# Kernel optimization log

Measured on AMD Instinct MI355X. Metric: run time of the kernel, lower is better.

The kernel has to match this reference:

```python
import jax, jax.numpy as jnp
import numpy as np

NB = 4096      # num_batch
NUM = 128      # trajectory samples (P rows)
NVAR = 16      # polynomial coeffs (P cols)
NOBS = 10      # obstacles
NL, NU = 4, 8  # num_lower, num_upper
NPART = NU - NL
T_FIN = 10.0
A_OBS, B_OBS = 6.0, 3.2
RHO_INEQ = RHO_OBS = RHO_LANE = 1.0
V_MIN, V_MAX, A_MAX = 0.1, 30.0, 18.0
MAXITER = 30
W_SM = 100.0


def setup_inputs() -> dict:
    key = jax.random.key(0)
    ks = jax.random.split(key, 13)
    f = jnp.float32
    return {
        'P': jax.random.normal(ks[0], (NUM, NVAR), f),
        'Pdot': jax.random.normal(ks[1], (NUM, NVAR), f),
        'Pddot': jax.random.normal(ks[2], (NUM, NVAR), f),
        'init_state_ego': jax.random.normal(ks[3], (NB, 4), f),
        'fin_state_ego': jax.random.normal(ks[4], (NB, 3), f),
        'closest_obs': jax.random.normal(ks[5], (NB, 2 * NOBS), f),
        'v_obs': jax.random.normal(ks[6], (NB, 2 * NOBS), f),
        'y_ub': jax.random.uniform(ks[7], (NB,), f),
        'y_lb': jax.random.normal(ks[8], (NB,), f),
        'lamda_x': jax.random.normal(ks[9], (NB, NVAR), f),
        'lamda_y': jax.random.normal(ks[10], (NB, NVAR), f),
        'c_x_partial': jax.random.normal(ks[11], (NB, NPART), f),
        'c_y_partial': jax.random.normal(ks[12], (NB, NPART), f),
    }


def _forward(P, Pdot, Pddot, init_state_ego, fin_state_ego, closest_obs, v_obs,
             y_ub, y_lb, lamda_x, lamda_y, c_x_partial, c_y_partial):
    num, nvar = P.shape
    tot_time = jnp.linspace(0.0, T_FIN, num)
    eye = jnp.eye(nvar, dtype=P.dtype)
    A_part = eye[NL:NU]
    A_eq_x = jnp.vstack([P[0], Pdot[0], Pddot[0], Pdot[-1], A_part])            # [4+NPART, nvar]
    A_eq_y = jnp.vstack([P[0], Pdot[0], Pddot[0], P[-1], Pdot[-1], A_part])     # [5+NPART, nvar]
    cost_sm = W_SM * (Pddot.T @ Pddot + 0.1 * eye)
    A_vel, A_acc = Pdot, Pddot
    A_obs_mat = jnp.tile(P, (NOBS, 1))            # [NOBS*num, nvar]
    A_lane = jnp.vstack([P, -P])                  # [2*num, nvar]

    def kkt_inv(cost, A_eq):
        m = A_eq.shape[0]
        top = jnp.hstack([cost, A_eq.T])
        bot = jnp.hstack([A_eq, jnp.zeros((m, m), cost.dtype)])
        return jnp.linalg.inv(jnp.vstack([top, bot]))

    # --- obstacle trajectories: [B, NOBS*num] ---
    x_obs = closest_obs[:, :NOBS]; y_obs = closest_obs[:, NOBS:2 * NOBS]
    vx_obs = v_obs[:, :NOBS];      vy_obs = v_obs[:, NOBS:2 * NOBS]
    x_obs_traj = (x_obs[:, :, None] + vx_obs[:, :, None] * tot_time).reshape(NB, NOBS * num)
    y_obs_traj = (y_obs[:, :, None] + vy_obs[:, :, None] * tot_time).reshape(NB, NOBS * num)

    # --- boundary vectors ---
    x_init = init_state_ego[:, 0:1]; y_init = init_state_ego[:, 1:2]
    v_init = init_state_ego[:, 2:3]; psi_init = init_state_ego[:, 3:4]
    vx_init = v_init * jnp.cos(psi_init); vy_init = v_init * jnp.sin(psi_init)
    zc = jnp.zeros((NB, 1), P.dtype)
    x_fin = fin_state_ego[:, 0:1]; y_fin = fin_state_ego[:, 1:2]
    vx_fin = jnp.clip(fin_state_ego[:, 2:3], V_MIN, V_MAX)  # computed as in original (unused in b_eq)
    b_eq_x = jnp.hstack([x_init, vx_init, zc, x_fin, c_x_partial])
    b_eq_y = jnp.hstack([y_init, vy_init, zc, y_fin, zc, c_y_partial])

    # --- initialization QP (lincost = 0) ---
    cmi_x0 = kkt_inv(cost_sm, A_eq_x)
    cmi_y0 = kkt_inv(cost_sm, A_eq_y)
    sol_x0 = jnp.hstack([jnp.zeros((NB, nvar), P.dtype), b_eq_x]) @ cmi_x0.T
    sol_y0 = jnp.hstack([jnp.zeros((NB, nvar), P.dtype), b_eq_y]) @ cmi_y0.T
    primal_sol = jnp.hstack([sol_x0[:, :nvar], sol_y0[:, :nvar]])

    # --- optimizer KKT inverses ---
    cost_x = cost_sm + RHO_INEQ * (A_acc.T @ A_acc) + RHO_INEQ * (A_vel.T @ A_vel) + RHO_OBS * (A_obs_mat.T @ A_obs_mat)
    cost_y = cost_x + RHO_LANE * (A_lane.T @ A_lane)
    cmi_x = kkt_inv(cost_x, A_eq_x)
    cmi_y = kkt_inv(cost_y, A_eq_y)

    ones_num = jnp.ones((NB, num), P.dtype)
    b_lane = jnp.hstack([y_ub[:, None] * ones_num, -y_lb[:, None] * ones_num])  # [B, 2*num]

    def step(carry, _):
        primal, lx, ly = carry
        cx, cy = primal[:, :nvar], primal[:, nvar:]
        x, xdot, xddot = cx @ P.T, cx @ Pdot.T, cx @ Pddot.T      # [B, num]
        y, ydot, yddot = cy @ P.T, cy @ Pdot.T, cy @ Pddot.T

        wc = jnp.tile(x, (1, NOBS)) - x_obs_traj                   # [B, NOBS*num]
        ws = jnp.tile(y, (1, NOBS)) - y_obs_traj
        alpha_obs = jnp.arctan2(ws * A_OBS, wc * B_OBS)
        co, so = jnp.cos(alpha_obs), jnp.sin(alpha_obs)
        c1 = RHO_OBS * (A_OBS ** 2 * co ** 2 + B_OBS ** 2 * so ** 2)
        c2 = RHO_OBS * (A_OBS * wc * co + B_OBS * ws * so)
        d_obs = jnp.maximum(1.0, c2 / c1)

        alpha_v = jnp.arctan2(ydot, xdot)
        cv, sv = jnp.cos(alpha_v), jnp.sin(alpha_v)
        d_v = jnp.clip(RHO_INEQ * (xdot * cv + ydot * sv) / (RHO_INEQ * (cv ** 2 + sv ** 2)), V_MIN, V_MAX)

        alpha_a = jnp.arctan2(yddot, xddot)
        ca, sa = jnp.cos(alpha_a), jnp.sin(alpha_a)
        d_a = jnp.clip(RHO_INEQ * (xddot * ca + yddot * sa) / (RHO_INEQ * (ca ** 2 + sa ** 2)), 0.0, A_MAX)

        Ay = cy @ A_lane.T                                         # [B, 2*num]
        s_lane = jnp.maximum(0.0, -Ay + b_lane)
        res_lane = Ay - b_lane + s_lane
        res_ax, res_ay = xddot - d_a * ca, yddot - d_a * sa
        res_vx, res_vy = xdot - d_v * cv, ydot - d_v * sv
        res_xo, res_yo = wc - A_OBS * d_obs * co, ws - B_OBS * d_obs * so

        lx = lx - RHO_INEQ * (res_ax @ A_acc) - RHO_INEQ * (res_vx @ A_vel) - RHO_OBS * (res_xo @ A_obs_mat)
        ly = ly - RHO_INEQ * (res_ay @ A_acc) - RHO_INEQ * (res_vy @ A_vel) \
                - RHO_OBS * (res_yo @ A_obs_mat) - RHO_LANE * (res_lane @ A_lane)

        tmp_xo = x_obs_traj + A_OBS * d_obs * co
        tmp_yo = y_obs_traj + B_OBS * d_obs * so
        lincost_x = -lx - RHO_OBS * (tmp_xo @ A_obs_mat) - RHO_INEQ * ((d_a * ca) @ A_acc) - RHO_INEQ * ((d_v * cv) @ A_vel)
        lincost_y = -ly - RHO_OBS * (tmp_yo @ A_obs_mat) - RHO_INEQ * ((d_a * sa) @ A_acc) - RHO_INEQ * ((d_v * sv) @ A_vel) \
                    - RHO_LANE * ((b_lane - s_lane) @ A_lane)
        sol_x = jnp.hstack([-lincost_x, b_eq_x]) @ cmi_x.T
        sol_y = jnp.hstack([-lincost_y, b_eq_y]) @ cmi_y.T
        primal = jnp.hstack([sol_x[:, :nvar], sol_y[:, :nvar]])
        return (primal, lx, ly), None

    (primal_sol, lamda_x, lamda_y), _ = jax.lax.scan(step, (primal_sol, lamda_x, lamda_y), None, length=MAXITER)
    return primal_sol


def reference(P, Pdot, Pddot, init_state_ego, fin_state_ego, closest_obs, v_obs,
              y_ub, y_lb, lamda_x, lamda_y, c_x_partial, c_y_partial):
    return _forward(P, Pdot, Pddot, init_state_ego, fin_state_ego, closest_obs, v_obs,
                    y_ub, y_lb, lamda_x, lamda_y, c_x_partial, c_y_partial)
```

## Files before the change

kernel.cpp:

```cpp
#include <hip/hip_runtime.h>
#include <math.h>

#define NBATCH 4096
#define TNUM   128
#define NOBSC  10
#define MAXIT  30

#define WS_MX   0
#define WS_MY   256
#define WS_MGX  512
#define WS_MGY  768
#define WS_NX   1024
#define WS_NY   1152
#define WS_NX0  1296
#define WS_NY0  1424

#define RSTRIDE 132

union F4 { float4 v; float f[4]; };

__global__ __launch_bounds__(64) void planner_setup(
    const float* __restrict__ P, const float* __restrict__ Pd, const float* __restrict__ Pdd,
    float* __restrict__ ws)
{
  const int mid = blockIdx.x;
  const int tid = threadIdx.x;
  __shared__ double C[16][16];
  __shared__ double G[16][16];
  __shared__ double Ae[9][16];
  __shared__ double aug[25][50];
  __shared__ int pivs;

  const bool isY = (mid & 1);
  const int  m   = isY ? 9 : 8;
  const int  n   = 16 + m;
  const int  w   = 2 * n;

  for (int e = tid; e < 256; e += 64) {
    const int j = e >> 4, k = e & 15;
    double gdd = 0.0, gd = 0.0, g0 = 0.0;
    for (int t = 0; t < TNUM; ++t) {
      gdd += (double)Pdd[t*16+j] * (double)Pdd[t*16+k];
      gd  += (double)Pd [t*16+j] * (double)Pd [t*16+k];
      g0  += (double)P  [t*16+j] * (double)P  [t*16+k];
    }
    const double cs = 100.0 * (gdd + ((j == k) ? 0.1 : 0.0));
    const double g  = gdd + gd + (isY ? 12.0 : 10.0) * g0;
    G[j][k] = g;
    C[j][k] = (mid >= 2) ? (cs + g) : cs;
  }
  if (tid < 16) {
    const int j = tid;
    Ae[0][j] = (double)P  [0*16+j];
    Ae[1][j] = (double)Pd [0*16+j];
    Ae[2][j] = (double)Pdd[0*16+j];
    if (!isY) {
      Ae[3][j] = (double)Pd[127*16+j];
      for (int r = 4; r < 8; ++r) Ae[r][j] = (j == r) ? 1.0 : 0.0;
    } else {
      Ae[3][j] = (double)P [127*16+j];
      Ae[4][j] = (double)Pd[127*16+j];
      for (int r = 5; r < 9; ++r) Ae[r][j] = (j == (r-1)) ? 1.0 : 0.0;
    }
  }
  __syncthreads();

  for (int e = tid; e < n * w; e += 64) {
    const int r = e / w, c = e % w;
    double val;
    if (c < n) {
      if (r < 16) val = (c < 16) ? C[r][c] : Ae[c-16][r];
      else        val = (c < 16) ? Ae[r-16][c] : 0.0;
    } else {
      val = ((c - n) == r) ? 1.0 : 0.0;
    }
    aug[r][c] = val;
  }
  __syncthreads();

  for (int k = 0; k < n; ++k) {
    if (tid == 0) {
      int p = k; double best = fabs(aug[k][k]);
      for (int r = k+1; r < n; ++r) { double a = fabs(aug[r][k]); if (a > best) { best = a; p = r; } }
      pivs = p;
    }
    __syncthreads();
    const int p = pivs;
    if (p != k) {
      for (int c = tid; c < w; c += 64) { double t = aug[k][c]; aug[k][c] = aug[p][c]; aug[p][c] = t; }
    }
    __syncthreads();
    const double ipiv = 1.0 / aug[k][k];
    for (int c = tid; c < w; c += 64) aug[k][c] *= ipiv;
    __syncthreads();
    for (int r = tid; r < n; r += 64) {
      if (r != k) {
        const double f = aug[r][k];
        for (int c = k; c < w; ++c) aug[r][c] -= f * aug[k][c];
      }
    }
    __syncthreads();
  }

  if (mid == 0) {
    for (int e = tid; e < 16*8; e += 64) ws[WS_NX0 + e] = (float)aug[e >> 3][n + 16 + (e & 7)];
  } else if (mid == 1) {
    for (int e = tid; e < 16*9; e += 64) ws[WS_NY0 + e] = (float)aug[e / 9][n + 16 + (e % 9)];
  } else if (mid == 2) {
    for (int e = tid; e < 256;  e += 64) ws[WS_MX + e] = (float)aug[e >> 4][n + (e & 15)];
    for (int e = tid; e < 16*8; e += 64) ws[WS_NX + e] = (float)aug[e >> 3][n + 16 + (e & 7)];
  } else {
    for (int e = tid; e < 256;  e += 64) ws[WS_MY + e] = (float)aug[e >> 4][n + (e & 15)];
    for (int e = tid; e < 16*9; e += 64) ws[WS_NY + e] = (float)aug[e / 9][n + 16 + (e % 9)];
  }

  if (mid >= 2) {
    for (int e = tid; e < 256; e += 64) {
      const int j = e >> 4, k = e & 15;
      double s = 0.0;
      for (int mm = 0; mm < 16; ++mm) s += aug[j][n + mm] * G[mm][k];
      ws[(mid == 2 ? WS_MGX : WS_MGY) + e] = (float)s;
    }
  }
}

__global__ __launch_bounds__(128) void planner_main(
    const float* __restrict__ P, const float* __restrict__ Pd, const float* __restrict__ Pdd,
    const float* __restrict__ init_state, const float* __restrict__ fin_state,
    const float* __restrict__ cobs, const float* __restrict__ vobs,
    const float* __restrict__ yub_g, const float* __restrict__ ylb_g,
    const float* __restrict__ lamx_g, const float* __restrict__ lamy_g,
    const float* __restrict__ cxp_g, const float* __restrict__ cyp_g,
    const float* __restrict__ ws, float* __restrict__ out)
{
  const int b    = blockIdx.x;
  const int tid  = threadIdx.x;
  const int lane = tid & 63;
  const int wv   = tid >> 6;
  const int r32  = lane & 31;
  const int rr   = tid & 15;
  const int side = (tid >> 4) & 1;

  __shared__ alignas(16) float red[32*RSTRIDE];
  __shared__ alignas(16) float cLw[2][32];
  __shared__ alignas(16) float hLw[2][32];
  __shared__ float pL[2][32];

  float Pr[16], Pdr[16], Pddr[16];
  #pragma unroll
  for (int q = 0; q < 4; ++q) {
    const float4 a  = *reinterpret_cast<const float4*>(P   + tid*16 + 4*q);
    const float4 bb = *reinterpret_cast<const float4*>(Pd  + tid*16 + 4*q);
    const float4 cc = *reinterpret_cast<const float4*>(Pdd + tid*16 + 4*q);
    Pr  [4*q+0]=a.x;  Pr  [4*q+1]=a.y;  Pr  [4*q+2]=a.z;  Pr  [4*q+3]=a.w;
    Pdr [4*q+0]=bb.x; Pdr [4*q+1]=bb.y; Pdr [4*q+2]=bb.z; Pdr [4*q+3]=bb.w;
    Pddr[4*q+0]=cc.x; Pddr[4*q+1]=cc.y; Pddr[4*q+2]=cc.z; Pddr[4*q+3]=cc.w;
  }

  float xot32[10], yot6[10];
  {
    const float tt = (float)tid * (10.0f/127.0f);
    #pragma unroll
    for (int oo = 0; oo < NOBSC; ++oo) {
      xot32[oo] = 3.2f * fmaf(vobs[b*20+oo],      tt, cobs[b*20+oo]);
      yot6 [oo] = 6.0f * fmaf(vobs[b*20+10+oo],   tt, cobs[b*20+10+oo]);
    }
  }
  const float yub = yub_g[b], ylb = ylb_g[b];

  float lam, constv, myc;
  {
    float beq[9];
    const float vi  = init_state[b*4+2];
    const float psi = init_state[b*4+3];
    if (side == 0) {
      beq[0] = init_state[b*4+0];
      beq[1] = vi * cosf(psi);
      beq[2] = 0.f;
      beq[3] = fin_state[b*3+0];
      #pragma unroll
      for (int i2 = 0; i2 < 4; ++i2) beq[4+i2] = cxp_g[b*4+i2];
      beq[8] = 0.f;
    } else {
      beq[0] = init_state[b*4+1];
      beq[1] = vi * sinf(psi);
      beq[2] = 0.f;
      beq[3] = fin_state[b*3+1];
      beq[4] = 0.f;
      #pragma unroll
      for (int i2 = 0; i2 < 4; ++i2) beq[5+i2] = cyp_g[b*4+i2];
    }
    const int nstr = side ? 9 : 8;
    const float* Np  = ws + (side ? WS_NY  : WS_NX ) + rr*nstr;
    const float* N0p = ws + (side ? WS_NY0 : WS_NX0) + rr*nstr;
    float cv = 0.f, c0 = 0.f;
    #pragma unroll
    for (int mm = 0; mm < 9; ++mm) {
      const float bm = beq[mm];
      cv = fmaf(Np[mm],  bm, cv);
      c0 = fmaf(N0p[mm], bm, c0);
    }
    constv = cv;
    myc    = c0;
    lam = (side == 0) ? lamx_g[b*16 + rr] : lamy_g[b*16 + rr];
    if (lane < 32) cLw[wv][lane] = c0;
  }

  const float* Mrow  = ws + (side ? WS_MY  : WS_MX ) + rr*16;
  const float* MGrow = ws + (side ? WS_MGY : WS_MGX) + rr*16;

  #pragma unroll 1
  for (int it = 0; it < MAXIT; ++it) {
    float x=0.f, y=0.f, xd=0.f, yd=0.f, xdd=0.f, ydd=0.f;
    #pragma unroll
    for (int q = 0; q < 4; ++q) {
      F4 cx4, cy4;
      cx4.v = *reinterpret_cast<const float4*>(&cLw[wv][4*q]);
      cy4.v = *reinterpret_cast<const float4*>(&cLw[wv][16 + 4*q]);
      #pragma unroll
      for (int j = 0; j < 4; ++j) {
        const int jj = 4*q + j;
        const float cc = cx4.f[j], dd = cy4.f[j];
        x   = fmaf(Pr  [jj], cc, x);   y   = fmaf(Pr  [jj], dd, y);
        xd  = fmaf(Pdr [jj], cc, xd);  yd  = fmaf(Pdr [jj], dd, yd);
        xdd = fmaf(Pddr[jj], cc, xdd); ydd = fmaf(Pddr[jj], dd, ydd);
      }
    }

    const float ria = rsqrtf(fmaxf(fmaf(xdd, xdd, ydd*ydd), 1e-36f));
    const float ga1 = 1.0f - fminf(1.0f, 18.0f * ria);
    const float riv = rsqrtf(fmaxf(fmaf(xd, xd, yd*yd), 1e-36f));
    const float gv1 = 1.0f - fminf(fmaxf(1.0f, 0.1f*riv), 30.0f*riv);

    float Sxp = 0.f, Syp = 0.f;
    #pragma unroll
    for (int oo = 0; oo < NOBSC; ++oo) {
      const float bw = fmaf(3.2f, x, -xot32[oo]);
      const float aw = fmaf(6.0f, y, -yot6[oo]);
      const float ri = rsqrtf(fmaxf(fmaf(bw, bw, aw*aw), 1e-36f));
      const float e  = fmaxf(fmaf(19.2f, ri, -1.0f), 0.f);
      Sxp = fmaf(e, bw, Sxp);
      Syp = fmaf(e, aw, Syp);
    }
    const float c0p = -Sxp * 0.3125f;
    const float rln = fmaxf(y - yub, 0.f) - fmaxf(ylb - y, 0.f);
    const float c2p = rln - Syp * (1.0f/6.0f);
    const float c0dd = xdd * ga1, c0d = xd * gv1;
    const float c2dd = ydd * ga1, c2d = yd * gv1;

    {
      float* col = red + tid;
      #pragma unroll
      for (int j = 0; j < 16; ++j) {
        col[j*RSTRIDE]      = fmaf(c0dd, Pddr[j], fmaf(c0d, Pdr[j], c0p * Pr[j]));
        col[(16+j)*RSTRIDE] = fmaf(c2dd, Pddr[j], fmaf(c2d, Pdr[j], c2p * Pr[j]));
      }
    }
    __syncthreads();

    {
      const int qq = tid >> 5;
      const float* rb = red + r32*RSTRIDE + qq*32;
      float s0=0.f, s1=0.f, s2=0.f, s3=0.f;
      #pragma unroll
      for (int mch = 0; mch < 8; ++mch) {
        const float4 t = *reinterpret_cast<const float4*>(rb + 4*mch);
        s0 += t.x; s1 += t.y; s2 += t.z; s3 += t.w;
      }
      float s = (s0 + s1) + (s2 + s3);
      s += __shfl_xor(s, 32);
      if (lane < 32) pL[wv][lane] = s;
      __syncthreads();

      const float S = s + pL[wv ^ 1][r32];
      lam -= S;
      const float h = lam - S;
      if (lane < 32) hLw[wv][lane] = h;
    }

    {
      float acc = constv;
      #pragma unroll
      for (int q = 0; q < 4; ++q) {
        F4 m4, g4, h4, c4;
        m4.v = *reinterpret_cast<const float4*>(Mrow  + 4*q);
        g4.v = *reinterpret_cast<const float4*>(MGrow + 4*q);
        h4.v = *reinterpret_cast<const float4*>(&hLw[wv][side*16 + 4*q]);
        c4.v = *reinterpret_cast<const float4*>(&cLw[wv][side*16 + 4*q]);
        #pragma unroll
        for (int j = 0; j < 4; ++j)
          acc = fmaf(g4.f[j], c4.f[j], fmaf(m4.f[j], h4.f[j], acc));
      }
      myc = acc;
      if (lane < 32) cLw[wv][lane] = acc;
    }
  }

  if (tid < 32) out[b*32 + tid] = myc;
}

extern "C" void kernel_launch(void* const* d_in, const int* in_sizes, int n_in,
                              void* d_out, int out_size, void* d_ws, size_t ws_size,
                              hipStream_t stream) {
  const float* P    = (const float*)d_in[0];
  const float* Pd   = (const float*)d_in[1];
  const float* Pdd  = (const float*)d_in[2];
  const float* init = (const float*)d_in[3];
  const float* fin  = (const float*)d_in[4];
  const float* cobs = (const float*)d_in[5];
  const float* vobs = (const float*)d_in[6];
  const float* yub  = (const float*)d_in[7];
  const float* ylb  = (const float*)d_in[8];
  const float* lamx = (const float*)d_in[9];
  const float* lamy = (const float*)d_in[10];
  const float* cxp  = (const float*)d_in[11];
  const float* cyp  = (const float*)d_in[12];
  float* ws  = (float*)d_ws;
  float* o   = (float*)d_out;

  planner_setup<<<dim3(4), dim3(64), 0, stream>>>(P, Pd, Pdd, ws);
  planner_main<<<dim3(NBATCH), dim3(128), 0, stream>>>(
      P, Pd, Pdd, init, fin, cobs, vobs, yub, ylb, lamx, lamy, cxp, cyp, ws, o);
}
```

Before: 246.1 us.

## Run each batch on a single wavefront with packed FMA and DPP reductions

The main kernel now uses one 64-thread wavefront per batch instead of two, with each thread handling two trajectory samples. __syncthreads is replaced by wave barriers. Packed 2-wide FMAs are used for the polynomial evaluations and obstacle terms, and the 32-row projection reduction is done with DPP quad sums followed by a much smaller shared buffer. This removes block-level barriers and most LDS traffic, but doubles per-thread work and register pressure and adds select logic.

```diff
diff --git a/kernel.cpp b/kernel.cpp
--- a/kernel.cpp
+++ b/kernel.cpp
@@ -15,9 +15,22 @@
 #define WS_NX0  1296
 #define WS_NY0  1424
 
-#define RSTRIDE 132
-
+#define RS 36
+
+typedef float f32x2 __attribute__((ext_vector_type(2)));
 union F4 { float4 v; float f[4]; };
+
+__device__ __forceinline__ f32x2 pfma(f32x2 a, f32x2 b, f32x2 c) {
+  return __builtin_elementwise_fma(a, b, c);
+}
+
+__device__ __forceinline__ float qsum(float v) {
+  float s = v + __int_as_float(__builtin_amdgcn_update_dpp(
+      0, __float_as_int(v), 0xB1, 0xF, 0xF, true));
+  s = s + __int_as_float(__builtin_amdgcn_update_dpp(
+      0, __float_as_int(s), 0x4E, 0xF, 0xF, true));
+  return s;
+}
 
 __global__ __launch_bounds__(64) void planner_setup(
     const float* __restrict__ P, const float* __restrict__ Pd, const float* __restrict__ Pdd,
@@ -37,17 +50,17 @@
   const int  w   = 2 * n;
 
   for (int e = tid; e < 256; e += 64) {
-    const int j = e >> 4, k = e & 15;
+    const int j = e >> 4, kk = e & 15;
     double gdd = 0.0, gd = 0.0, g0 = 0.0;
     for (int t = 0; t < TNUM; ++t) {
-      gdd += (double)Pdd[t*16+j] * (double)Pdd[t*16+k];
-      gd  += (double)Pd [t*16+j] * (double)Pd [t*16+k];
-      g0  += (double)P  [t*16+j] * (double)P  [t*16+k];
-    }
-    const double cs = 100.0 * (gdd + ((j == k) ? 0.1 : 0.0));
+      gdd += (double)Pdd[t*16+j] * (double)Pdd[t*16+kk];
+      gd  += (double)Pd [t*16+j] * (double)Pd [t*16+kk];
+      g0  += (double)P  [t*16+j] * (double)P  [t*16+kk];
+    }
+    const double cs = 100.0 * (gdd + ((j == kk) ? 0.1 : 0.0));
     const double g  = gdd + gd + (isY ? 12.0 : 10.0) * g0;
-    G[j][k] = g;
-    C[j][k] = (mid >= 2) ? (cs + g) : cs;
+    G[j][kk] = g;
+    C[j][kk] = (mid >= 2) ? (cs + g) : cs;
   }
   if (tid < 16) {
     const int j = tid;
@@ -78,25 +91,25 @@
   }
   __syncthreads();
 
-  for (int k = 0; k < n; ++k) {
+  for (int kk = 0; kk < n; ++kk) {
     if (tid == 0) {
-      int p = k; double best = fabs(aug[k][k]);
-      for (int r = k+1; r < n; ++r) { double a = fabs(aug[r][k]); if (a > best) { best = a; p = r; } }
+      int p = kk; double best = fabs(aug[kk][kk]);
+      for (int r = kk+1; r < n; ++r) { double a = fabs(aug[r][kk]); if (a > best) { best = a; p = r; } }
       pivs = p;
     }
     __syncthreads();
     const int p = pivs;
-    if (p != k) {
-      for (int c = tid; c < w; c += 64) { double t = aug[k][c]; aug[k][c] = aug[p][c]; aug[p][c] = t; }
+    if (p != kk) {
+      for (int c = tid; c < w; c += 64) { double t = aug[kk][c]; aug[kk][c] = aug[p][c]; aug[p][c] = t; }
     }
     __syncthreads();
-    const double ipiv = 1.0 / aug[k][k];
-    for (int c = tid; c < w; c += 64) aug[k][c] *= ipiv;
+    const double ipiv = 1.0 / aug[kk][kk];
+    for (int c = tid; c < w; c += 64) aug[kk][c] *= ipiv;
     __syncthreads();
     for (int r = tid; r < n; r += 64) {
-      if (r != k) {
-        const double f = aug[r][k];
-        for (int c = k; c < w; ++c) aug[r][c] -= f * aug[k][c];
+      if (r != kk) {
+        const double f = aug[r][kk];
+        for (int c = kk; c < w; ++c) aug[r][c] -= f * aug[kk][c];
       }
     }
     __syncthreads();
@@ -116,15 +129,15 @@
 
   if (mid >= 2) {
     for (int e = tid; e < 256; e += 64) {
-      const int j = e >> 4, k = e & 15;
+      const int j = e >> 4, kk = e & 15;
       double s = 0.0;
-      for (int mm = 0; mm < 16; ++mm) s += aug[j][n + mm] * G[mm][k];
+      for (int mm = 0; mm < 16; ++mm) s += aug[j][n + mm] * G[mm][kk];
       ws[(mid == 2 ? WS_MGX : WS_MGY) + e] = (float)s;
     }
   }
 }
 
-__global__ __launch_bounds__(128) void planner_main(
+__global__ __launch_bounds__(64) void planner_main(
     const float* __restrict__ P, const float* __restrict__ Pd, const float* __restrict__ Pdd,
     const float* __restrict__ init_state, const float* __restrict__ fin_state,
     const float* __restrict__ cobs, const float* __restrict__ vobs,
@@ -135,40 +148,55 @@
 {
   const int b    = blockIdx.x;
   const int tid  = threadIdx.x;
-  const int lane = tid & 63;
-  const int wv   = tid >> 6;
-  const int r32  = lane & 31;
+  const int o32  = tid & 31;
+  const int cc   = tid >> 5;
   const int rr   = tid & 15;
   const int side = (tid >> 4) & 1;
-
-  __shared__ alignas(16) float red[32*RSTRIDE];
-  __shared__ alignas(16) float cLw[2][32];
-  __shared__ alignas(16) float hLw[2][32];
-  __shared__ float pL[2][32];
-
-  float Pr[16], Pdr[16], Pddr[16];
+  const int q4   = tid >> 2;
+  const int k    = tid & 3;
+
+  __shared__ alignas(16) float red[16*RS];
+  __shared__ alignas(16) float cL[32];
+  __shared__ alignas(16) float hL[32];
+
+  f32x2 Pr2[2][8], Pdr2[2][8], Pddr2[2][8];
   #pragma unroll
-  for (int q = 0; q < 4; ++q) {
-    const float4 a  = *reinterpret_cast<const float4*>(P   + tid*16 + 4*q);
-    const float4 bb = *reinterpret_cast<const float4*>(Pd  + tid*16 + 4*q);
-    const float4 cc = *reinterpret_cast<const float4*>(Pdd + tid*16 + 4*q);
-    Pr  [4*q+0]=a.x;  Pr  [4*q+1]=a.y;  Pr  [4*q+2]=a.z;  Pr  [4*q+3]=a.w;
-    Pdr [4*q+0]=bb.x; Pdr [4*q+1]=bb.y; Pdr [4*q+2]=bb.z; Pdr [4*q+3]=bb.w;
-    Pddr[4*q+0]=cc.x; Pddr[4*q+1]=cc.y; Pddr[4*q+2]=cc.z; Pddr[4*q+3]=cc.w;
-  }
-
-  float xot32[10], yot6[10];
+  for (int u = 0; u < 2; ++u) {
+    const int t = tid + 64*u;
+    #pragma unroll
+    for (int q = 0; q < 4; ++q) {
+      F4 a, bb, ce;
+      a.v  = *reinterpret_cast<const float4*>(P   + t*16 + 4*q);
+      bb.v = *reinterpret_cast<const float4*>(Pd  + t*16 + 4*q);
+      ce.v = *reinterpret_cast<const float4*>(Pdd + t*16 + 4*q);
+      Pr2  [u][2*q+0] = f32x2{a.f[0],  a.f[1]};  Pr2  [u][2*q+1] = f32x2{a.f[2],  a.f[3]};
+      Pdr2 [u][2*q+0] = f32x2{bb.f[0], bb.f[1]}; Pdr2 [u][2*q+1] = f32x2{bb.f[2], bb.f[3]};
+      Pddr2[u][2*q+0] = f32x2{ce.f[0], ce.f[1]}; Pddr2[u][2*q+1] = f32x2{ce.f[2], ce.f[3]};
+    }
+  }
+
+  f32x2 xot0[5], yot0[5], xot1[5], yot1[5];
   {
-    const float tt = (float)tid * (10.0f/127.0f);
+    const float tt0 = (float)tid        * (10.0f/127.0f);
+    const float tt1 = (float)(tid + 64) * (10.0f/127.0f);
     #pragma unroll
-    for (int oo = 0; oo < NOBSC; ++oo) {
-      xot32[oo] = 3.2f * fmaf(vobs[b*20+oo],      tt, cobs[b*20+oo]);
-      yot6 [oo] = 6.0f * fmaf(vobs[b*20+10+oo],   tt, cobs[b*20+10+oo]);
+    for (int o5 = 0; o5 < 5; ++o5) {
+      const int o = 2*o5;
+      const float xo0 = cobs[b*20+o],    xo1 = cobs[b*20+o+1];
+      const float yo0 = cobs[b*20+10+o], yo1 = cobs[b*20+11+o];
+      const float vx0 = vobs[b*20+o],    vx1 = vobs[b*20+o+1];
+      const float vy0 = vobs[b*20+10+o], vy1 = vobs[b*20+11+o];
+      xot0[o5] = f32x2{3.2f*fmaf(vx0,tt0,xo0), 3.2f*fmaf(vx1,tt0,xo1)};
+      yot0[o5] = f32x2{6.0f*fmaf(vy0,tt0,yo0), 6.0f*fmaf(vy1,tt0,yo1)};
+      xot1[o5] = f32x2{3.2f*fmaf(vx0,tt1,xo0), 3.2f*fmaf(vx1,tt1,xo1)};
+      yot1[o5] = f32x2{6.0f*fmaf(vy0,tt1,yo0), 6.0f*fmaf(vy1,tt1,yo1)};
     }
   }
   const float yub = yub_g[b], ylb = ylb_g[b];
 
-  float lam, constv, myc;
+  float lam = (o32 < 16) ? lamx_g[b*16 + o32] : lamy_g[b*16 + (o32 - 16)];
+
+  float constv, myc;
   {
     float beq[9];
     const float vi  = init_state[b*4+2];
@@ -202,98 +230,148 @@
     }
     constv = cv;
     myc    = c0;
-    lam = (side == 0) ? lamx_g[b*16 + rr] : lamy_g[b*16 + rr];
-    if (lane < 32) cLw[wv][lane] = c0;
-  }
+  }
+  if (tid < 32) cL[tid] = myc;
 
   const float* Mrow  = ws + (side ? WS_MY  : WS_MX ) + rr*16;
   const float* MGrow = ws + (side ? WS_MGY : WS_MGX) + rr*16;
+  const bool  kb2 = (k & 2) != 0;
+  const int   k1  = k & 1;
 
   #pragma unroll 1
   for (int it = 0; it < MAXIT; ++it) {
-    float x=0.f, y=0.f, xd=0.f, yd=0.f, xdd=0.f, ydd=0.f;
+    __builtin_amdgcn_wave_barrier();
+    f32x2 xv0{},yv0{},xdv0{},ydv0{},xddv0{},yddv0{};
+    f32x2 xv1{},yv1{},xdv1{},ydv1{},xddv1{},yddv1{};
     #pragma unroll
     for (int q = 0; q < 4; ++q) {
       F4 cx4, cy4;
-      cx4.v = *reinterpret_cast<const float4*>(&cLw[wv][4*q]);
-      cy4.v = *reinterpret_cast<const float4*>(&cLw[wv][16 + 4*q]);
-      #pragma unroll
-      for (int j = 0; j < 4; ++j) {
-        const int jj = 4*q + j;
-        const float cc = cx4.f[j], dd = cy4.f[j];
-        x   = fmaf(Pr  [jj], cc, x);   y   = fmaf(Pr  [jj], dd, y);
-        xd  = fmaf(Pdr [jj], cc, xd);  yd  = fmaf(Pdr [jj], dd, yd);
-        xdd = fmaf(Pddr[jj], cc, xdd); ydd = fmaf(Pddr[jj], dd, ydd);
+      cx4.v = *reinterpret_cast<const float4*>(&cL[4*q]);
+      cy4.v = *reinterpret_cast<const float4*>(&cL[16 + 4*q]);
+      const f32x2 c01 = f32x2{cx4.f[0], cx4.f[1]}, c23 = f32x2{cx4.f[2], cx4.f[3]};
+      const f32x2 d01 = f32x2{cy4.f[0], cy4.f[1]}, d23 = f32x2{cy4.f[2], cy4.f[3]};
+      xv0   = pfma(Pr2  [0][2*q], c01, xv0);   xv0   = pfma(Pr2  [0][2*q+1], c23, xv0);
+      yv0   = pfma(Pr2  [0][2*q], d01, yv0);   yv0   = pfma(Pr2  [0][2*q+1], d23, yv0);
+      xdv0  = pfma(Pdr2 [0][2*q], c01, xdv0);  xdv0  = pfma(Pdr2 [0][2*q+1], c23, xdv0);
+      ydv0  = pfma(Pdr2 [0][2*q], d01, ydv0);  ydv0  = pfma(Pdr2 [0][2*q+1], d23, ydv0);
+      xddv0 = pfma(Pddr2[0][2*q], c01, xddv0); xddv0 = pfma(Pddr2[0][2*q+1], c23, xddv0);
+      yddv0 = pfma(Pddr2[0][2*q], d01, yddv0); yddv0 = pfma(Pddr2[0][2*q+1], d23, yddv0);
+      xv1   = pfma(Pr2  [1][2*q], c01, xv1);   xv1   = pfma(Pr2  [1][2*q+1], c23, xv1);
+      yv1   = pfma(Pr2  [1][2*q], d01, yv1);   yv1   = pfma(Pr2  [1][2*q+1], d23, yv1);
+      xdv1  = pfma(Pdr2 [1][2*q], c01, xdv1);  xdv1  = pfma(Pdr2 [1][2*q+1], c23, xdv1);
+      ydv1  = pfma(Pdr2 [1][2*q], d01, ydv1);  ydv1  = pfma(Pdr2 [1][2*q+1], d23, ydv1);
+      xddv1 = pfma(Pddr2[1][2*q], c01, xddv1); xddv1 = pfma(Pddr2[1][2*q+1], c23, xddv1);
+      yddv1 = pfma(Pddr2[1][2*q], d01, yddv1); yddv1 = pfma(Pddr2[1][2*q+1], d23, yddv1);
+    }
+    const float x0=xv0.x+xv0.y, y0=yv0.x+yv0.y, xd0=xdv0.x+xdv0.y, yd0=ydv0.x+ydv0.y;
+    const float xdd0=xddv0.x+xddv0.y, ydd0=yddv0.x+yddv0.y;
+    const float x1=xv1.x+xv1.y, y1=yv1.x+yv1.y, xd1=xdv1.x+xdv1.y, yd1=ydv1.x+ydv1.y;
+    const float xdd1=xddv1.x+xddv1.y, ydd1=yddv1.x+yddv1.y;
+
+    const float ria0 = rsqrtf(fmaxf(fmaf(xdd0,xdd0,ydd0*ydd0), 1e-36f));
+    const float ga10 = 1.0f - fminf(1.0f, 18.0f*ria0);
+    const float riv0 = rsqrtf(fmaxf(fmaf(xd0,xd0,yd0*yd0), 1e-36f));
+    const float gv10 = 1.0f - fminf(fmaxf(1.0f, 0.1f*riv0), 30.0f*riv0);
+    const float ria1 = rsqrtf(fmaxf(fmaf(xdd1,xdd1,ydd1*ydd1), 1e-36f));
+    const float ga11 = 1.0f - fminf(1.0f, 18.0f*ria1);
+    const float riv1 = rsqrtf(fmaxf(fmaf(xd1,xd1,yd1*yd1), 1e-36f));
+    const float gv11 = 1.0f - fminf(fmaxf(1.0f, 0.1f*riv1), 30.0f*riv1);
+
+    f32x2 Sx0{}, Sy0{}, Sx1{}, Sy1{};
+    {
+      const f32x2 xb0 = f32x2{3.2f*x0, 3.2f*x0}, yb0 = f32x2{6.0f*y0, 6.0f*y0};
+      const f32x2 xb1 = f32x2{3.2f*x1, 3.2f*x1}, yb1 = f32x2{6.0f*y1, 6.0f*y1};
+      #pragma unroll
+      for (int o5 = 0; o5 < 5; ++o5) {
+        const f32x2 bw0 = xb0 - xot0[o5], aw0 = yb0 - yot0[o5];
+        const f32x2 bw1 = xb1 - xot1[o5], aw1 = yb1 - yot1[o5];
+        const f32x2 r20 = pfma(bw0,bw0,aw0*aw0);
+        const f32x2 r21 = pfma(bw1,bw1,aw1*aw1);
+        const f32x2 ee0 = f32x2{
+          fmaxf(fmaf(19.2f, rsqrtf(fmaxf(r20.x,1e-36f)), -1.0f), 0.f),
+          fmaxf(fmaf(19.2f, rsqrtf(fmaxf(r20.y,1e-36f)), -1.0f), 0.f)};
+        const f32x2 ee1 = f32x2{
+          fmaxf(fmaf(19.2f, rsqrtf(fmaxf(r21.x,1e-36f)), -1.0f), 0.f),
+          fmaxf(fmaf(19.2f, rsqrtf(fmaxf(r21.y,1e-36f)), -1.0f), 0.f)};
+        Sx0 = pfma(ee0, bw0, Sx0);  Sy0 = pfma(ee0, aw0, Sy0);
+        Sx1 = pfma(ee1, bw1, Sx1);  Sy1 = pfma(ee1, aw1, Sy1);
       }
     }
-
-    const float ria = rsqrtf(fmaxf(fmaf(xdd, xdd, ydd*ydd), 1e-36f));
-    const float ga1 = 1.0f - fminf(1.0f, 18.0f * ria);
-    const float riv = rsqrtf(fmaxf(fmaf(xd, xd, yd*yd), 1e-36f));
-    const float gv1 = 1.0f - fminf(fmaxf(1.0f, 0.1f*riv), 30.0f*riv);
-
-    float Sxp = 0.f, Syp = 0.f;
+    const float c0p0 = -(Sx0.x+Sx0.y)*0.3125f;
+    const float rln0 = fmaxf(y0-yub,0.f) - fmaxf(ylb-y0,0.f);
+    const float c2p0 = rln0 - (Sy0.x+Sy0.y)*(1.0f/6.0f);
+    const float c0dd0 = xdd0*ga10, c0d0 = xd0*gv10;
+    const float c2dd0 = ydd0*ga10, c2d0 = yd0*gv10;
+    const float c0p1 = -(Sx1.x+Sx1.y)*0.3125f;
+    const float rln1 = fmaxf(y1-yub,0.f) - fmaxf(ylb-y1,0.f);
+    const float c2p1 = rln1 - (Sy1.x+Sy1.y)*(1.0f/6.0f);
+    const float c0dd1 = xdd1*ga11, c0d1 = xd1*gv11;
+    const float c2dd1 = ydd1*ga11, c2d1 = yd1*gv11;
+
+    float outv[8];
     #pragma unroll
-    for (int oo = 0; oo < NOBSC; ++oo) {
-      const float bw = fmaf(3.2f, x, -xot32[oo]);
-      const float aw = fmaf(6.0f, y, -yot6[oo]);
-      const float ri = rsqrtf(fmaxf(fmaf(bw, bw, aw*aw), 1e-36f));
-      const float e  = fmaxf(fmaf(19.2f, ri, -1.0f), 0.f);
-      Sxp = fmaf(e, bw, Sxp);
-      Syp = fmaf(e, aw, Syp);
-    }
-    const float c0p = -Sxp * 0.3125f;
-    const float rln = fmaxf(y - yub, 0.f) - fmaxf(ylb - y, 0.f);
-    const float c2p = rln - Syp * (1.0f/6.0f);
-    const float c0dd = xdd * ga1, c0d = xd * gv1;
-    const float c2dd = ydd * ga1, c2d = yd * gv1;
-
+    for (int s2 = 0; s2 < 8; ++s2) outv[s2] = 0.f;
     {
-      float* col = red + tid;
-      #pragma unroll
-      for (int j = 0; j < 16; ++j) {
-        col[j*RSTRIDE]      = fmaf(c0dd, Pddr[j], fmaf(c0d, Pdr[j], c0p * Pr[j]));
-        col[(16+j)*RSTRIDE] = fmaf(c2dd, Pddr[j], fmaf(c2d, Pdr[j], c2p * Pr[j]));
+      const f32x2 A00{c0dd0,c0dd0}, D00{c0d0,c0d0}, Q00{c0p0,c0p0};
+      const f32x2 A20{c2dd0,c2dd0}, D20{c2d0,c2d0}, Q20{c2p0,c2p0};
+      const f32x2 A01{c0dd1,c0dd1}, D01{c0d1,c0d1}, Q01{c0p1,c0p1};
+      const f32x2 A21{c2dd1,c2dd1}, D21{c2d1,c2d1}, Q21{c2p1,c2p1};
+      #pragma unroll
+      for (int j2 = 0; j2 < 8; ++j2) {
+        f32x2 vx = pfma(A00, Pddr2[0][j2], pfma(D00, Pdr2[0][j2], Q00*Pr2[0][j2]));
+        vx = pfma(A01, Pddr2[1][j2], pfma(D01, Pdr2[1][j2], pfma(Q01, Pr2[1][j2], vx)));
+        f32x2 vy = pfma(A20, Pddr2[0][j2], pfma(D20, Pdr2[0][j2], Q20*Pr2[0][j2]));
+        vy = pfma(A21, Pddr2[1][j2], pfma(D21, Pdr2[1][j2], pfma(Q21, Pr2[1][j2], vy)));
+        const float qx0 = qsum(vx.x), qx1 = qsum(vx.y);
+        const float qy0 = qsum(vy.x), qy1 = qsum(vy.y);
+        const float s0 = kb2 ? qy0 : qx0;
+        const float s1 = kb2 ? qy1 : qx1;
+        const bool match = (k1 == (j2 >> 2));
+        const int  sb = 2*(j2 & 3);
+        outv[sb]   = match ? s0 : outv[sb];
+        outv[sb+1] = match ? s1 : outv[sb+1];
       }
     }
-    __syncthreads();
-
+    __builtin_amdgcn_wave_barrier();
     {
-      const int qq = tid >> 5;
-      const float* rb = red + r32*RSTRIDE + qq*32;
-      float s0=0.f, s1=0.f, s2=0.f, s3=0.f;
-      #pragma unroll
-      for (int mch = 0; mch < 8; ++mch) {
-        const float4 t = *reinterpret_cast<const float4*>(rb + 4*mch);
-        s0 += t.x; s1 += t.y; s2 += t.z; s3 += t.w;
-      }
-      float s = (s0 + s1) + (s2 + s3);
+      float* wr = red + q4*RS + 8*k;
+      *reinterpret_cast<float4*>(wr)     = float4{outv[0],outv[1],outv[2],outv[3]};
+      *reinterpret_cast<float4*>(wr + 4) = float4{outv[4],outv[5],outv[6],outv[7]};
+    }
+    __builtin_amdgcn_wave_barrier();
+
+    float h;
+    {
+      const float* rd = red + (cc*8)*RS + o32;
+      float s = 0.f;
+      #pragma unroll
+      for (int i = 0; i < 8; ++i) s += rd[i*RS];
       s += __shfl_xor(s, 32);
-      if (lane < 32) pL[wv][lane] = s;
-      __syncthreads();
-
-      const float S = s + pL[wv ^ 1][r32];
-      lam -= S;
-      const float h = lam - S;
-      if (lane < 32) hLw[wv][lane] = h;
-    }
+      lam -= s;
+      h = lam - s;
+    }
+    __builtin_amdgcn_wave_barrier();
+    if (tid < 32) hL[tid] = h;
+    __builtin_amdgcn_wave_barrier();
 
     {
-      float acc = constv;
+      f32x2 accv{};
       #pragma unroll
       for (int q = 0; q < 4; ++q) {
         F4 m4, g4, h4, c4;
         m4.v = *reinterpret_cast<const float4*>(Mrow  + 4*q);
         g4.v = *reinterpret_cast<const float4*>(MGrow + 4*q);
-        h4.v = *reinterpret_cast<const float4*>(&hLw[wv][side*16 + 4*q]);
-        c4.v = *reinterpret_cast<const float4*>(&cLw[wv][side*16 + 4*q]);
-        #pragma unroll
-        for (int j = 0; j < 4; ++j)
-          acc = fmaf(g4.f[j], c4.f[j], fmaf(m4.f[j], h4.f[j], acc));
+        h4.v = *reinterpret_cast<const float4*>(&hL[side*16 + 4*q]);
+        c4.v = *reinterpret_cast<const float4*>(&cL[side*16 + 4*q]);
+        accv = pfma(f32x2{m4.f[0],m4.f[1]}, f32x2{h4.f[0],h4.f[1]}, accv);
+        accv = pfma(f32x2{g4.f[0],g4.f[1]}, f32x2{c4.f[0],c4.f[1]}, accv);
+        accv = pfma(f32x2{m4.f[2],m4.f[3]}, f32x2{h4.f[2],h4.f[3]}, accv);
+        accv = pfma(f32x2{g4.f[2],g4.f[3]}, f32x2{c4.f[2],c4.f[3]}, accv);
       }
-      myc = acc;
-      if (lane < 32) cLw[wv][lane] = acc;
-    }
+      myc = constv + accv.x + accv.y;
+    }
+    __builtin_amdgcn_wave_barrier();
+    if (tid < 32) cL[tid] = myc;
   }
 
   if (tid < 32) out[b*32 + tid] = myc;
@@ -319,6 +397,6 @@
   float* o   = (float*)d_out;
 
   planner_setup<<<dim3(4), dim3(64), 0, stream>>>(P, Pd, Pdd, ws);
-  planner_main<<<dim3(NBATCH), dim3(128), 0, stream>>>(
+  planner_main<<<dim3(NBATCH), dim3(64), 0, stream>>>(
       P, Pd, Pdd, init, fin, cobs, vobs, yub, ylb, lamx, lamy, cxp, cyp, ws, o);
 }
```

After: 254.1 us. 3.2% more time.
